# Performance work log

Hardware: AMD Instinct MI355X
Metric: run time of the kernel (lower is better)

## Reference

```python
import jax, jax.numpy as jnp
import numpy as np

B, CH, D, H, W = 8, 64, 32, 64, 64
S = CH // 2  # shrink


def setup_inputs() -> dict:
    key = jax.random.key(0)
    ks = jax.random.split(key, 10)
    sc = 0.05
    x = jax.random.normal(ks[0], (B, CH, D, H, W), jnp.float32)
    Wk = jax.random.normal(ks[1], (S, CH), jnp.float32) * sc
    bk = jax.random.normal(ks[2], (S,), jnp.float32) * sc
    Wq = jax.random.normal(ks[3], (S, CH), jnp.float32) * sc
    bq = jax.random.normal(ks[4], (S,), jnp.float32) * sc
    Wv = jax.random.normal(ks[5], (S, CH), jnp.float32) * sc
    bv = jax.random.normal(ks[6], (S,), jnp.float32) * sc
    Wo = jax.random.normal(ks[7], (CH, S), jnp.float32) * sc
    bo = jax.random.normal(ks[8], (CH,), jnp.float32) * sc
    # original inits atten_factor to 0 (which zeroes the attention branch);
    # use a nonzero value so the attention path is exercised.
    factor = jnp.full((1,), 0.5, jnp.float32)
    return {"x": x, "Wk": Wk, "bk": bk, "Wq": Wq, "bq": bq,
            "Wv": Wv, "bv": bv, "Wo": Wo, "bo": bo, "factor": factor}


def reference(x, Wk, bk, Wq, bq, Wv, bv, Wo, bo, factor):
    b, c, d, h, w = x.shape
    s = Wk.shape[0]

    def proj(Wm, bm):
        # conv3d 1x1 + permute(0,3,4,1,2) fused: [B,C,D,H,W] -> [B,H,W,S,D]
        y = jnp.einsum('oc,bcdhw->bhwod', Wm, x) + bm[None, None, None, :, None]
        return y.reshape(b * h * w, s, d)

    k = proj(Wk, bk)
    q = proj(Wq, bq)
    v = proj(Wv, bv)
    # scores [N, D, D]; softmax over dim=1 (the k-derived axis), matching torch
    scores = jnp.einsum('nsi,nsj->nij', k, q) / jnp.sqrt(jnp.float32(s))
    a = jax.nn.softmax(scores, axis=1)
    o = jnp.einsum('nsd,ndj->nsj', v, a)                    # [N, S, D]
    o = o.reshape(b, h, w, s, d)
    # output conv1x1 back to C channels, layout [B,C,D,H,W]
    o = jnp.einsum('os,bhwsd->bodhw', Wo, o) + bo[None, :, None, None, None]
    y = x + factor[0] * o
    return jnp.mean(y, axis=2)                              # [B, C, H, W]
```

## Files before the change

### kernel.cpp

```cpp
#include <hip/hip_runtime.h>


namespace {
constexpr int kB = 8, kC = 64, kD = 32, kH = 64, kW = 64, kS = 32;
constexpr int TW = 8, NT = 256;
constexpr int XR = 72;
constexpr int VR = 36;
constexpr int QOFF = 40;

typedef unsigned short u16t;
typedef unsigned int u32t;
typedef __attribute__((ext_vector_type(8))) short bf16x8;
typedef __attribute__((ext_vector_type(4))) float f32x4;
typedef __attribute__((ext_vector_type(4))) short short4v;

__device__ __forceinline__ float b2f(u16t u) {
    union { u32t i; float f; } v; v.i = ((u32t)u) << 16; return v.f;
}
__device__ __forceinline__ u16t f2b(float f) {
    union { u32t i; float f; } v; v.f = f;
    u32t r = v.i + 0x7FFFu + ((v.i >> 16) & 1u);
    return (u16t)(r >> 16);
}
__device__ __forceinline__ bf16x8 pack8(const float4 f0, const float4 f1) {
    bf16x8 a;
    a[0] = (short)f2b(f0.x); a[1] = (short)f2b(f0.y);
    a[2] = (short)f2b(f0.z); a[3] = (short)f2b(f0.w);
    a[4] = (short)f2b(f1.x); a[5] = (short)f2b(f1.y);
    a[6] = (short)f2b(f1.z); a[7] = (short)f2b(f1.w);
    return a;
}
}

__global__ __launch_bounds__(NT, 2) void attn_fused(
    const float* __restrict__ x,
    const float* __restrict__ Wk, const float* __restrict__ bk,
    const float* __restrict__ Wq, const float* __restrict__ bq,
    const float* __restrict__ Wv, const float* __restrict__ bv,
    const float* __restrict__ Wo, const float* __restrict__ bo,
    const float* __restrict__ factor,
    float* __restrict__ out)
{
    __shared__ u16t KQX[256 * XR];
    __shared__ u16t VT[256 * VR];
    __shared__ float biasS[160];
    __shared__ float XbarS[kC * TW];
    __shared__ float AbarS[TW * 33];
    __shared__ float ObarS[TW * 33];
    const int t = threadIdx.x;
    const int lane = t & 63;
    const int wv = t >> 6;
    const int l15 = lane & 15;
    const int quad = lane >> 4;

    const int blk = blockIdx.x;
    const int bh = (blk & 7) | ((blk >> 6) << 3);
    const int wt = (blk >> 3) & 7;
    const int b = bh >> 6, h = bh & 63, w0 = wt * TW;

    if (t < 32) { biasS[t] = bk[t]; biasS[32 + t] = bq[t]; biasS[64 + t] = bv[t]; }
    if (t < 64) { biasS[96 + t] = bo[t]; }

    {
        const float* xb = x + (size_t)(b * kC * kD) * (kH * kW) + h * kW + w0;
        u32t* dst = (u32t*)KQX;
        #pragma unroll
        for (int it = 0; it < 8; ++it) {
            int unit = it * NT + t;
            int w4 = unit & 1;
            int d  = (unit >> 1) & 31;
            int cp = unit >> 6;
            int c  = cp * 2;
            const float4 fa = *(const float4*)(xb + (size_t)(c * kD + d) * (kH * kW) + w4 * 4);
            const float4 fb = *(const float4*)(xb + (size_t)((c + 1) * kD + d) * (kH * kW) + w4 * 4);
            int r0 = (w4 * 4) * kD + d;
            dst[(r0 + 0 * kD) * 36 + cp] = (u32t)f2b(fa.x) | ((u32t)f2b(fb.x) << 16);
            dst[(r0 + 1 * kD) * 36 + cp] = (u32t)f2b(fa.y) | ((u32t)f2b(fb.y) << 16);
            dst[(r0 + 2 * kD) * 36 + cp] = (u32t)f2b(fa.z) | ((u32t)f2b(fb.z) << 16);
            dst[(r0 + 3 * kD) * 36 + cp] = (u32t)f2b(fa.w) | ((u32t)f2b(fb.w) << 16);
        }
    }
    __syncthreads();

    {
        int c = t & 63, wb = t >> 6;
        #pragma unroll
        for (int half = 0; half < 2; ++half) {
            int wp = wb + half * 4;
            const u16t* col = &KQX[(wp * kD) * XR + c];
            float s = 0.f;
            #pragma unroll
            for (int d = 0; d < kD; ++d) s += b2f(col[d * XR]);
            XbarS[c * TW + wp] = s * (1.0f / kD);
        }
    }
    __syncthreads();

    {
        bf16x8 Bf[4][2];
        #pragma unroll
        for (int nt = 0; nt < 4; ++nt) {
            int row = wv * 64 + nt * 16 + l15;
            #pragma unroll
            for (int ks = 0; ks < 2; ++ks)
                Bf[nt][ks] = *(const bf16x8*)&KQX[row * XR + ks * 32 + quad * 8];
        }
        #pragma unroll
        for (int p = 0; p < 3; ++p) {
            const float* Wp = (p == 0) ? Wk : (p == 1) ? Wq : Wv;
            bf16x8 Af[2][2];
            #pragma unroll
            for (int m0 = 0; m0 < 2; ++m0)
                #pragma unroll
                for (int ks = 0; ks < 2; ++ks) {
                    const float* src = Wp + (m0 * 16 + l15) * kC + ks * 32 + quad * 8;
                    Af[m0][ks] = pack8(*(const float4*)src, *(const float4*)(src + 4));
                }
            float bvv[2][4];
            #pragma unroll
            for (int m0 = 0; m0 < 2; ++m0)
                #pragma unroll
                for (int r2 = 0; r2 < 4; ++r2)
                    bvv[m0][r2] = biasS[p * 32 + m0 * 16 + quad * 4 + r2];
            #pragma unroll
            for (int m0 = 0; m0 < 2; ++m0) {
                #pragma unroll
                for (int nt = 0; nt < 4; ++nt) {
                    f32x4 acc = {0.f, 0.f, 0.f, 0.f};
                    acc = __builtin_amdgcn_mfma_f32_16x16x32_bf16(Af[m0][0], Bf[nt][0], acc, 0, 0, 0);
                    acc = __builtin_amdgcn_mfma_f32_16x16x32_bf16(Af[m0][1], Bf[nt][1], acc, 0, 0, 0);
                    int row = wv * 64 + nt * 16 + l15;
                    short4v pk;
                    pk.x = (short)f2b(acc[0] + bvv[m0][0]);
                    pk.y = (short)f2b(acc[1] + bvv[m0][1]);
                    pk.z = (short)f2b(acc[2] + bvv[m0][2]);
                    pk.w = (short)f2b(acc[3] + bvv[m0][3]);
                    if (p < 2) {
                        *(short4v*)&KQX[row * XR + (p == 0 ? 0 : QOFF) + m0 * 16 + quad * 4] = pk;
                    } else {
                        *(short4v*)&VT[row * VR + m0 * 16 + quad * 4] = pk;
                    }
                }
            }
        }
    }
    __syncthreads();

    {
        const float scale = 0.17677669529663687f;
        #pragma unroll
        for (int si = 0; si < 2; ++si) {
            int wp = wv * 2 + si;
            bf16x8 Ka[2], Qb[2];
            #pragma unroll
            for (int m0 = 0; m0 < 2; ++m0)
                Ka[m0] = *(const bf16x8*)&KQX[(wp * kD + m0 * 16 + l15) * XR + quad * 8];
            #pragma unroll
            for (int n0 = 0; n0 < 2; ++n0)
                Qb[n0] = *(const bf16x8*)&KQX[(wp * kD + n0 * 16 + l15) * XR + QOFF + quad * 8];
            f32x4 sc[2][2];
            #pragma unroll
            for (int m0 = 0; m0 < 2; ++m0)
                #pragma unroll
                for (int n0 = 0; n0 < 2; ++n0) {
                    f32x4 z = {0.f, 0.f, 0.f, 0.f};
                    sc[m0][n0] = __builtin_amdgcn_mfma_f32_16x16x32_bf16(Ka[m0], Qb[n0], z, 0, 0, 0);
                }
            #pragma unroll
            for (int n0 = 0; n0 < 2; ++n0) {
                float m = sc[0][n0][0];
                #pragma unroll
                for (int m0 = 0; m0 < 2; ++m0)
                    #pragma unroll
                    for (int r2 = 0; r2 < 4; ++r2) m = fmaxf(m, sc[m0][n0][r2]);
                m = fmaxf(m, __shfl_xor(m, 16));
                m = fmaxf(m, __shfl_xor(m, 32));
                float sum = 0.f;
                #pragma unroll
                for (int m0 = 0; m0 < 2; ++m0)
                    #pragma unroll
                    for (int r2 = 0; r2 < 4; ++r2) {
                        float e = __expf((sc[m0][n0][r2] - m) * scale);
                        sc[m0][n0][r2] = e; sum += e;
                    }
                sum += __shfl_xor(sum, 16);
                sum += __shfl_xor(sum, 32);
                float inv = 1.0f / sum;
                #pragma unroll
                for (int m0 = 0; m0 < 2; ++m0)
                    #pragma unroll
                    for (int r2 = 0; r2 < 4; ++r2) sc[m0][n0][r2] *= inv;
            }
            #pragma unroll
            for (int m0 = 0; m0 < 2; ++m0)
                #pragma unroll
                for (int r2 = 0; r2 < 4; ++r2) {
                    float v2 = sc[m0][0][r2] + sc[m0][1][r2];
                    v2 += __shfl_xor(v2, 1);
                    v2 += __shfl_xor(v2, 2);
                    v2 += __shfl_xor(v2, 4);
                    v2 += __shfl_xor(v2, 8);
                    if (l15 == 0)
                        AbarS[wp * 33 + m0 * 16 + quad * 4 + r2] = v2 * (1.0f / kD);
                }
        }
    }
    __syncthreads();

    {
        int s = t & 31, wp = (t >> 5) & 7;
        const u16t* vcol = &VT[(wp * kD) * VR + s];
        const float* ab = &AbarS[wp * 33];
        float acc = 0.f;
        #pragma unroll
        for (int d = 0; d < kD; ++d) acc += b2f(vcol[d * VR]) * ab[d];
        ObarS[wp * 33 + s] = acc;
    }
    __syncthreads();

    {
        const float fac = factor[0];
        int wp = t & 7, cl = t >> 3;
        #pragma unroll
        for (int half = 0; half < 2; ++half) {
            int c = cl + half * 32;
            const float* wrow = Wo + c * kS;
            const float* ob = &ObarS[wp * 33];
            float acc = 0.f;
            #pragma unroll
            for (int s2 = 0; s2 < kS; ++s2) acc += wrow[s2] * ob[s2];
            out[((b * kC + c) * kH + h) * kW + w0 + wp] =
                XbarS[c * TW + wp] + fac * (biasS[96 + c] + acc);
        }
    }
}

extern "C" void kernel_launch(void* const* d_in, const int* in_sizes, int n_in,
                              void* d_out, int out_size, void* d_ws, size_t ws_size,
                              hipStream_t stream) {
    const float* x      = (const float*)d_in[0];
    const float* Wk     = (const float*)d_in[1];
    const float* bk     = (const float*)d_in[2];
    const float* Wq     = (const float*)d_in[3];
    const float* bq     = (const float*)d_in[4];
    const float* Wv     = (const float*)d_in[5];
    const float* bv     = (const float*)d_in[6];
    const float* Wo     = (const float*)d_in[7];
    const float* bo     = (const float*)d_in[8];
    const float* factor = (const float*)d_in[9];
    float* out = (float*)d_out;

    dim3 grid(kB * kH * (kW / TW));
    attn_fused<<<grid, NT, 0, stream>>>(x, Wk, bk, Wq, bq, Wv, bv, Wo, bo, factor, out);
}
```

Measured before the change: 449.7 us.

## Keep V in registers, fuse means into MFMA fragments, drop syncs and LDS buffers

Computes the depth mean of x from the already-loaded MFMA B fragments using lane shuffles instead of a separate LDS pass, keeps the V projection in registers and reduces it against the averaged attention right after the softmax, and removes the VT and bias LDS buffers along with two barriers. It also reorders the global load mapping so consecutive threads walk channel pairs, vectorises the Wo dot product, and raises launch bounds to target four blocks per CU. The aim is to cut LDS traffic, barrier stalls and shared-memory footprint so occupancy rises, at the cost of more shuffles and more register pressure.

```diff
diff --git a/kernel.cpp b/kernel.cpp
--- a/kernel.cpp
+++ b/kernel.cpp
@@ -5,7 +5,6 @@
 constexpr int kB = 8, kC = 64, kD = 32, kH = 64, kW = 64, kS = 32;
 constexpr int TW = 8, NT = 256;
 constexpr int XR = 72;
-constexpr int VR = 36;
 constexpr int QOFF = 40;
 
 typedef unsigned short u16t;
@@ -21,6 +20,9 @@
     union { u32t i; float f; } v; v.f = f;
     u32t r = v.i + 0x7FFFu + ((v.i >> 16) & 1u);
     return (u16t)(r >> 16);
+}
+__device__ __forceinline__ u32t pack2(float lo, float hi) {
+    return (u32t)f2b(lo) | ((u32t)f2b(hi) << 16);
 }
 __device__ __forceinline__ bf16x8 pack8(const float4 f0, const float4 f1) {
     bf16x8 a;
@@ -32,7 +34,7 @@
 }
 }
 
-__global__ __launch_bounds__(NT, 2) void attn_fused(
+__global__ __launch_bounds__(NT, 4) void attn_fused(
     const float* __restrict__ x,
     const float* __restrict__ Wk, const float* __restrict__ bk,
     const float* __restrict__ Wq, const float* __restrict__ bq,
@@ -41,12 +43,10 @@
     const float* __restrict__ factor,
     float* __restrict__ out)
 {
-    __shared__ u16t KQX[256 * XR];
-    __shared__ u16t VT[256 * VR];
-    __shared__ float biasS[160];
+    __shared__ __align__(16) u16t KQX[256 * XR];
     __shared__ float XbarS[kC * TW];
-    __shared__ float AbarS[TW * 33];
-    __shared__ float ObarS[TW * 33];
+    __shared__ float AbarS[TW * kD];
+    __shared__ float ObarS[kS * TW];
     const int t = threadIdx.x;
     const int lane = t & 63;
     const int wv = t >> 6;
@@ -58,9 +58,6 @@
     const int wt = (blk >> 3) & 7;
     const int b = bh >> 6, h = bh & 63, w0 = wt * TW;
 
-    if (t < 32) { biasS[t] = bk[t]; biasS[32 + t] = bq[t]; biasS[64 + t] = bv[t]; }
-    if (t < 64) { biasS[96 + t] = bo[t]; }
-
     {
         const float* xb = x + (size_t)(b * kC * kD) * (kH * kW) + h * kW + w0;
         u32t* dst = (u32t*)KQX;
@@ -68,83 +65,95 @@
         for (int it = 0; it < 8; ++it) {
             int unit = it * NT + t;
             int w4 = unit & 1;
-            int d  = (unit >> 1) & 31;
-            int cp = unit >> 6;
+            int cp = (unit >> 1) & 31;
+            int d  = unit >> 6;
             int c  = cp * 2;
             const float4 fa = *(const float4*)(xb + (size_t)(c * kD + d) * (kH * kW) + w4 * 4);
             const float4 fb = *(const float4*)(xb + (size_t)((c + 1) * kD + d) * (kH * kW) + w4 * 4);
             int r0 = (w4 * 4) * kD + d;
-            dst[(r0 + 0 * kD) * 36 + cp] = (u32t)f2b(fa.x) | ((u32t)f2b(fb.x) << 16);
-            dst[(r0 + 1 * kD) * 36 + cp] = (u32t)f2b(fa.y) | ((u32t)f2b(fb.y) << 16);
-            dst[(r0 + 2 * kD) * 36 + cp] = (u32t)f2b(fa.z) | ((u32t)f2b(fb.z) << 16);
-            dst[(r0 + 3 * kD) * 36 + cp] = (u32t)f2b(fa.w) | ((u32t)f2b(fb.w) << 16);
+            dst[(r0 + 0 * kD) * 36 + cp] = pack2(fa.x, fb.x);
+            dst[(r0 + 1 * kD) * 36 + cp] = pack2(fa.y, fb.y);
+            dst[(r0 + 2 * kD) * 36 + cp] = pack2(fa.z, fb.z);
+            dst[(r0 + 3 * kD) * 36 + cp] = pack2(fa.w, fb.w);
         }
     }
     __syncthreads();
 
-    {
-        int c = t & 63, wb = t >> 6;
-        #pragma unroll
-        for (int half = 0; half < 2; ++half) {
-            int wp = wb + half * 4;
-            const u16t* col = &KQX[(wp * kD) * XR + c];
-            float s = 0.f;
-            #pragma unroll
-            for (int d = 0; d < kD; ++d) s += b2f(col[d * XR]);
-            XbarS[c * TW + wp] = s * (1.0f / kD);
-        }
-    }
-    __syncthreads();
-
-    {
-        bf16x8 Bf[4][2];
-        #pragma unroll
-        for (int nt = 0; nt < 4; ++nt) {
-            int row = wv * 64 + nt * 16 + l15;
+    bf16x8 Bf[4][2];
+    #pragma unroll
+    for (int nt = 0; nt < 4; ++nt) {
+        int row = wv * 64 + nt * 16 + l15;
+        #pragma unroll
+        for (int ks = 0; ks < 2; ++ks)
+            Bf[nt][ks] = *(const bf16x8*)&KQX[row * XR + ks * 32 + quad * 8];
+    }
+
+    #pragma unroll
+    for (int hh = 0; hh < 2; ++hh) {
+        float xb16[16];
+        #pragma unroll
+        for (int ks = 0; ks < 2; ++ks)
+            #pragma unroll
+            for (int e = 0; e < 8; ++e)
+                xb16[ks * 8 + e] = b2f((u16t)Bf[hh * 2 + 0][ks][e])
+                                 + b2f((u16t)Bf[hh * 2 + 1][ks][e]);
+        #pragma unroll
+        for (int i = 0; i < 16; ++i) {
+            float v = xb16[i];
+            v += __shfl_xor(v, 1);
+            v += __shfl_xor(v, 2);
+            v += __shfl_xor(v, 4);
+            v += __shfl_xor(v, 8);
+            xb16[i] = v;
+        }
+        if (l15 == 0) {
             #pragma unroll
             for (int ks = 0; ks < 2; ++ks)
-                Bf[nt][ks] = *(const bf16x8*)&KQX[row * XR + ks * 32 + quad * 8];
-        }
-        #pragma unroll
-        for (int p = 0; p < 3; ++p) {
-            const float* Wp = (p == 0) ? Wk : (p == 1) ? Wq : Wv;
-            bf16x8 Af[2][2];
-            #pragma unroll
-            for (int m0 = 0; m0 < 2; ++m0)
-                #pragma unroll
-                for (int ks = 0; ks < 2; ++ks) {
-                    const float* src = Wp + (m0 * 16 + l15) * kC + ks * 32 + quad * 8;
-                    Af[m0][ks] = pack8(*(const float4*)src, *(const float4*)(src + 4));
-                }
-            float bvv[2][4];
-            #pragma unroll
-            for (int m0 = 0; m0 < 2; ++m0)
-                #pragma unroll
-                for (int r2 = 0; r2 < 4; ++r2)
-                    bvv[m0][r2] = biasS[p * 32 + m0 * 16 + quad * 4 + r2];
-            #pragma unroll
-            for (int m0 = 0; m0 < 2; ++m0) {
-                #pragma unroll
-                for (int nt = 0; nt < 4; ++nt) {
-                    f32x4 acc = {0.f, 0.f, 0.f, 0.f};
-                    acc = __builtin_amdgcn_mfma_f32_16x16x32_bf16(Af[m0][0], Bf[nt][0], acc, 0, 0, 0);
-                    acc = __builtin_amdgcn_mfma_f32_16x16x32_bf16(Af[m0][1], Bf[nt][1], acc, 0, 0, 0);
+                #pragma unroll
+                for (int e = 0; e < 8; ++e) {
+                    int c = ks * 32 + quad * 8 + e;
+                    XbarS[c * TW + 2 * wv + hh] = xb16[ks * 8 + e] * (1.0f / kD);
+                }
+        }
+    }
+
+    short4v Vp[2][4];
+    #pragma unroll
+    for (int p = 0; p < 3; ++p) {
+        const float* Wp = (p == 0) ? Wk : (p == 1) ? Wq : Wv;
+        const float* bp = (p == 0) ? bk : (p == 1) ? bq : bv;
+        bf16x8 Af[2][2];
+        float4 bias4[2];
+        #pragma unroll
+        for (int m0 = 0; m0 < 2; ++m0) {
+            #pragma unroll
+            for (int ks = 0; ks < 2; ++ks) {
+                const float* src = Wp + (m0 * 16 + l15) * kC + ks * 32 + quad * 8;
+                Af[m0][ks] = pack8(*(const float4*)src, *(const float4*)(src + 4));
+            }
+            bias4[m0] = *(const float4*)(bp + m0 * 16 + quad * 4);
+        }
+        #pragma unroll
+        for (int m0 = 0; m0 < 2; ++m0) {
+            #pragma unroll
+            for (int nt = 0; nt < 4; ++nt) {
+                f32x4 acc = {0.f, 0.f, 0.f, 0.f};
+                acc = __builtin_amdgcn_mfma_f32_16x16x32_bf16(Af[m0][0], Bf[nt][0], acc, 0, 0, 0);
+                acc = __builtin_amdgcn_mfma_f32_16x16x32_bf16(Af[m0][1], Bf[nt][1], acc, 0, 0, 0);
+                short4v pk;
+                pk.x = (short)f2b(acc[0] + bias4[m0].x);
+                pk.y = (short)f2b(acc[1] + bias4[m0].y);
+                pk.z = (short)f2b(acc[2] + bias4[m0].z);
+                pk.w = (short)f2b(acc[3] + bias4[m0].w);
+                if (p < 2) {
                     int row = wv * 64 + nt * 16 + l15;
-                    short4v pk;
-                    pk.x = (short)f2b(acc[0] + bvv[m0][0]);
-                    pk.y = (short)f2b(acc[1] + bvv[m0][1]);
-                    pk.z = (short)f2b(acc[2] + bvv[m0][2]);
-                    pk.w = (short)f2b(acc[3] + bvv[m0][3]);
-                    if (p < 2) {
-                        *(short4v*)&KQX[row * XR + (p == 0 ? 0 : QOFF) + m0 * 16 + quad * 4] = pk;
-                    } else {
-                        *(short4v*)&VT[row * VR + m0 * 16 + quad * 4] = pk;
-                    }
-                }
-            }
-        }
-    }
-    __syncthreads();
+                    *(short4v*)&KQX[row * XR + (p == 0 ? 0 : QOFF) + m0 * 16 + quad * 4] = pk;
+                } else {
+                    Vp[m0][nt] = pk;
+                }
+            }
+        }
+    }
 
     {
         const float scale = 0.17677669529663687f;
@@ -201,20 +210,26 @@
                     v2 += __shfl_xor(v2, 4);
                     v2 += __shfl_xor(v2, 8);
                     if (l15 == 0)
-                        AbarS[wp * 33 + m0 * 16 + quad * 4 + r2] = v2 * (1.0f / kD);
-                }
-        }
-    }
-    __syncthreads();
-
-    {
-        int s = t & 31, wp = (t >> 5) & 7;
-        const u16t* vcol = &VT[(wp * kD) * VR + s];
-        const float* ab = &AbarS[wp * 33];
-        float acc = 0.f;
-        #pragma unroll
-        for (int d = 0; d < kD; ++d) acc += b2f(vcol[d * VR]) * ab[d];
-        ObarS[wp * 33 + s] = acc;
+                        AbarS[wp * kD + m0 * 16 + quad * 4 + r2] = v2 * (1.0f / kD);
+                }
+            {
+                float ab0 = AbarS[wp * kD + l15];
+                float ab1 = AbarS[wp * kD + 16 + l15];
+                #pragma unroll
+                for (int m0 = 0; m0 < 2; ++m0)
+                    #pragma unroll
+                    for (int r2 = 0; r2 < 4; ++r2) {
+                        float v = b2f((u16t)Vp[m0][2 * si + 0][r2]) * ab0
+                                + b2f((u16t)Vp[m0][2 * si + 1][r2]) * ab1;
+                        v += __shfl_xor(v, 1);
+                        v += __shfl_xor(v, 2);
+                        v += __shfl_xor(v, 4);
+                        v += __shfl_xor(v, 8);
+                        if (l15 == 0)
+                            ObarS[(m0 * 16 + quad * 4 + r2) * TW + wp] = v;
+                    }
+            }
+        }
     }
     __syncthreads();
 
@@ -224,13 +239,18 @@
         #pragma unroll
         for (int half = 0; half < 2; ++half) {
             int c = cl + half * 32;
-            const float* wrow = Wo + c * kS;
-            const float* ob = &ObarS[wp * 33];
+            const float4* wrow = (const float4*)(Wo + c * kS);
             float acc = 0.f;
             #pragma unroll
-            for (int s2 = 0; s2 < kS; ++s2) acc += wrow[s2] * ob[s2];
+            for (int s4 = 0; s4 < 8; ++s4) {
+                float4 w4 = wrow[s4];
+                acc += w4.x * ObarS[(s4 * 4 + 0) * TW + wp];
+                acc += w4.y * ObarS[(s4 * 4 + 1) * TW + wp];
+                acc += w4.z * ObarS[(s4 * 4 + 2) * TW + wp];
+                acc += w4.w * ObarS[(s4 * 4 + 3) * TW + wp];
+            }
             out[((b * kC + c) * kH + h) * kW + w0 + wp] =
-                XbarS[c * TW + wp] + fac * (biasS[96 + c] + acc);
+                XbarS[c * TW + wp] + fac * (bo[c] + acc);
         }
     }
 }
```

Result: faster. 431.5 us (-4.1%).
